# Kernel optimization log

Measured on AMD Instinct MI355X. Metric: run time of the kernel, lower is better.

## Reference

```python
import jax, jax.numpy as jnp
import numpy as np

NQ = 4          # n_qubits -> 2**4 = 16 amplitudes
NL = 3          # n_layers
TWO_PI = 2.0 * np.pi
BN_EPS = 1e-5


def _ry_batched(t):
    # t: [B] -> [B,2,2] complex64
    c, s = jnp.cos(t / 2), jnp.sin(t / 2)
    g = jnp.stack([jnp.stack([c, -s], -1), jnp.stack([s, c], -1)], -2)
    return g.astype(jnp.complex64)


def _ry(t):
    c, s = jnp.cos(t / 2), jnp.sin(t / 2)
    return jnp.stack([jnp.stack([c, -s]), jnp.stack([s, c])]).astype(jnp.complex64)


def _rz(t):
    e = jnp.stack([jnp.exp(-0.5j * t), jnp.exp(0.5j * t)]).astype(jnp.complex64)
    return jnp.diag(e)


def _apply_1q(state, gate, wire, batched):
    # state: [B,2,2,2,2]; gate: [2,2] or [B,2,2]
    s = jnp.moveaxis(state, wire + 1, -1)
    if batched:
        s = jnp.einsum('bij,b...j->b...i', gate, s)
    else:
        s = jnp.einsum('ij,...j->...i', gate, s)
    return jnp.moveaxis(s, -1, wire + 1)


def _apply_cnot(state, c, t):
    s = jnp.moveaxis(state, (c + 1, t + 1), (-2, -1))
    s = jnp.stack([s[..., 0, :], s[..., 1, ::-1]], axis=-2)  # flip target when control=1
    return jnp.moveaxis(s, (-2, -1), (c + 1, t + 1))


def _circuit(angles, weights):
    # angles: [B, NQ] float32; weights: [NL, NQ, 2]
    B = angles.shape[0]
    state = jnp.zeros((B,) + (2,) * NQ, jnp.complex64)
    state = state.at[(slice(None),) + (0,) * NQ].set(1.0)
    # input encoding RYs (per-sample angles -> batched gates)
    for i in range(NQ):
        state = _apply_1q(state, _ry_batched(angles[:, i]), i, True)
    for layer in range(NL):
        for i in range(NQ):
            state = _apply_1q(state, _ry(weights[layer, i, 0]), i, False)
            state = _apply_1q(state, _rz(weights[layer, i, 1]), i, False)
        for i in range(NQ - 1):
            state = _apply_cnot(state, i, i + 1)
        state = _apply_cnot(state, NQ - 1, 0)
    probs = jnp.abs(state) ** 2  # [B,2,2,2,2] real
    zs = []
    for i in range(NQ):
        axes = tuple(a for a in range(1, NQ + 1) if a != i + 1)
        pm = probs.sum(axis=axes)  # [B,2]
        zs.append(pm[:, 0] - pm[:, 1])
    return jnp.stack(zs, -1).astype(jnp.float32)  # [B,NQ]


def setup_inputs() -> dict:
    key = jax.random.key(0)
    ks = jax.random.split(key, 4)
    B = 524288
    x = jax.random.normal(ks[0], (B, 16), jnp.float32)
    weights = jax.random.normal(ks[1], (NL, NQ, 2), jnp.float32)
    fc_w = jax.random.normal(ks[2], (4, NQ), jnp.float32) / np.sqrt(NQ)
    fc_b = jax.random.normal(ks[3], (4,), jnp.float32) * 0.01
    gamma = jnp.ones((4,), jnp.float32)
    beta = jnp.zeros((4,), jnp.float32)
    return {"x": x, "weights": weights, "fc_w": fc_w, "fc_b": fc_b,
            "gamma": gamma, "beta": beta}


def reference(x, weights, fc_w, fc_b, gamma, beta):
    inp = x.reshape(x.shape[0], -1)[:, :NQ]
    mn, mx = inp.min(), inp.max()  # global min/max as in the torch code
    angles = TWO_PI * (inp - mn) / (mx - mn + 1e-8)
    q = _circuit(angles, weights)                # [B,4] PauliZ expvals
    out = q @ fc_w.T + fc_b                      # Linear(4,4)
    mean = out.mean(0)
    var = out.var(0)                             # biased, as torch BN training
    return gamma * (out - mean) / jnp.sqrt(var + BN_EPS) + beta
```

## Files before the change

kernel.cpp:

```cpp
#include <hip/hip_runtime.h>
#include <math.h>

#define TWO_PI_F 6.28318530717958647692f
#define BN_EPS_F 1e-5f


__device__ __forceinline__ unsigned f2key(float f) {
  unsigned u = __float_as_uint(f);
  return (u & 0x80000000u) ? ~u : (u | 0x80000000u);
}
__device__ __forceinline__ float key2f(unsigned k) {
  unsigned u = (k & 0x80000000u) ? (k ^ 0x80000000u) : ~k;
  return __uint_as_float(u);
}

__global__ void k_init(const float* __restrict__ w, float* __restrict__ wsf) {
  if (threadIdx.x == 0) {
    unsigned* wsu = (unsigned*)wsf;
    wsu[0] = 0xFFFFFFFFu;
    wsu[1] = 0x00000000u;
    for (int j = 0; j < 8; ++j) wsf[2 + j] = 0.0f;
    for (int l = 0; l < 3; ++l) {
      for (int i = 0; i < 4; ++i) {
        float th_ry = w[(l * 4 + i) * 2 + 0];
        float th_rz = w[(l * 4 + i) * 2 + 1];
        wsf[16 + l * 16 + i * 4 + 0] = cosf(0.5f * th_ry);
        wsf[16 + l * 16 + i * 4 + 1] = sinf(0.5f * th_ry);
        wsf[16 + l * 16 + i * 4 + 2] = cosf(0.5f * th_rz);
        wsf[16 + l * 16 + i * 4 + 3] = sinf(0.5f * th_rz);
      }
    }
  }
}

__global__ __launch_bounds__(256) void k_minmax(const float* __restrict__ x,
                                                unsigned* __restrict__ wsu, int B) {
  float fmn = __builtin_inff();
  float fmx = -__builtin_inff();
  for (int r = blockIdx.x * blockDim.x + threadIdx.x; r < B;
       r += gridDim.x * blockDim.x) {
    float4 v = *(const float4*)(x + (size_t)r * 16);
    fmn = fminf(fmn, fminf(fminf(v.x, v.y), fminf(v.z, v.w)));
    fmx = fmaxf(fmx, fmaxf(fmaxf(v.x, v.y), fmaxf(v.z, v.w)));
  }
#pragma unroll
  for (int d = 32; d; d >>= 1) {
    fmn = fminf(fmn, __shfl_down(fmn, d));
    fmx = fmaxf(fmx, __shfl_down(fmx, d));
  }
  __shared__ float smn[4], smx[4];
  int wave = threadIdx.x >> 6, lane = threadIdx.x & 63;
  if (lane == 0) { smn[wave] = fmn; smx[wave] = fmx; }
  __syncthreads();
  if (threadIdx.x == 0) {
    float bmn = fminf(fminf(smn[0], smn[1]), fminf(smn[2], smn[3]));
    float bmx = fmaxf(fmaxf(smx[0], smx[1]), fmaxf(smx[2], smx[3]));
    atomicMin(&wsu[0], f2key(bmn));
    atomicMax(&wsu[1], f2key(bmx));
  }
}

__global__ __launch_bounds__(256) void k_main(const float* __restrict__ x,
                                              const float* __restrict__ wsf,
                                              const float* __restrict__ fc_w,
                                              const float* __restrict__ fc_b,
                                              float* __restrict__ out, int B) {
  int b = blockIdx.x * 256 + threadIdx.x;
  const unsigned* wsu = (const unsigned*)wsf;
  float mn = key2f(wsu[0]);
  float mx = key2f(wsu[1]);
  float denom = mx - mn + 1e-8f;

  float o[4] = {0.f, 0.f, 0.f, 0.f};
  if (b < B) {
    float4 xv = *(const float4*)(x + (size_t)b * 16);
    float ang[4] = {TWO_PI_F * (xv.x - mn) / denom, TWO_PI_F * (xv.y - mn) / denom,
                    TWO_PI_F * (xv.z - mn) / denom, TWO_PI_F * (xv.w - mn) / denom};
    float cq[4], sq[4];
#pragma unroll
    for (int i = 0; i < 4; ++i) __sincosf(0.5f * ang[i], &sq[i], &cq[i]);

    float sr[16], si[16];
#pragma unroll
    for (int k = 0; k < 16; ++k) {
      sr[k] = ((k & 8) ? sq[0] : cq[0]) * ((k & 4) ? sq[1] : cq[1]) *
              ((k & 2) ? sq[2] : cq[2]) * ((k & 1) ? sq[3] : cq[3]);
      si[k] = 0.f;
    }

    const float* gt = wsf + 16;
#pragma unroll
    for (int l = 0; l < 3; ++l) {
#pragma unroll
      for (int i = 0; i < 4; ++i) {
        const int m = 8 >> i;
        float ryc = gt[l * 16 + i * 4 + 0];
        float rys = gt[l * 16 + i * 4 + 1];
        float rzc = gt[l * 16 + i * 4 + 2];
        float rzs = gt[l * 16 + i * 4 + 3];
#pragma unroll
        for (int k = 0; k < 16; ++k) {
          if (!(k & m)) {
            int k1 = k | m;
            float a0r = sr[k], a0i = si[k], a1r = sr[k1], a1i = si[k1];
            sr[k]  = ryc * a0r - rys * a1r;
            si[k]  = ryc * a0i - rys * a1i;
            sr[k1] = rys * a0r + ryc * a1r;
            si[k1] = rys * a0i + ryc * a1i;
          }
        }
#pragma unroll
        for (int k = 0; k < 16; ++k) {
          float ps = (k & m) ? rzs : -rzs;
          float r = sr[k], ii = si[k];
          sr[k] = r * rzc - ii * ps;
          si[k] = r * ps + ii * rzc;
        }
      }
#pragma unroll
      for (int c = 0; c < 4; ++c) {
        const int mc = 8 >> c;
        const int mt = 8 >> ((c + 1) & 3);
#pragma unroll
        for (int k = 0; k < 16; ++k) {
          if ((k & mc) && !(k & mt)) {
            int k2 = k | mt;
            float t;
            t = sr[k]; sr[k] = sr[k2]; sr[k2] = t;
            t = si[k]; si[k] = si[k2]; si[k2] = t;
          }
        }
      }
    }

    float z[4] = {0.f, 0.f, 0.f, 0.f};
#pragma unroll
    for (int k = 0; k < 16; ++k) {
      float p = sr[k] * sr[k] + si[k] * si[k];
#pragma unroll
      for (int i = 0; i < 4; ++i) z[i] += (k & (8 >> i)) ? -p : p;
    }
#pragma unroll
    for (int j = 0; j < 4; ++j) {
      float acc = fc_b[j];
#pragma unroll
      for (int i = 0; i < 4; ++i) acc += fc_w[j * 4 + i] * z[i];
      o[j] = acc;
    }
    *(float4*)(out + (size_t)b * 4) = make_float4(o[0], o[1], o[2], o[3]);
  }

  float vals[8] = {o[0], o[1], o[2], o[3],
                   o[0] * o[0], o[1] * o[1], o[2] * o[2], o[3] * o[3]};
#pragma unroll
  for (int j = 0; j < 8; ++j) {
#pragma unroll
    for (int d = 32; d; d >>= 1) vals[j] += __shfl_down(vals[j], d);
  }
  __shared__ float red[4][8];
  int wave = threadIdx.x >> 6, lane = threadIdx.x & 63;
  if (lane == 0) {
#pragma unroll
    for (int j = 0; j < 8; ++j) red[wave][j] = vals[j];
  }
  __syncthreads();
  if (threadIdx.x < 8) {
    float s = red[0][threadIdx.x] + red[1][threadIdx.x] + red[2][threadIdx.x] +
              red[3][threadIdx.x];
    float* stats = (float*)wsf + 2;
    atomicAdd(&stats[threadIdx.x], s);
  }
}

__global__ __launch_bounds__(256) void k_final(float* __restrict__ out,
                                               const float* __restrict__ wsf,
                                               const float* __restrict__ gamma,
                                               const float* __restrict__ beta, int B) {
  int b = blockIdx.x * 256 + threadIdx.x;
  if (b >= B) return;
  const float* stats = wsf + 2;
  float inv = 1.0f / (float)B;
  float4 v = *(float4*)(out + (size_t)b * 4);
  float vv[4] = {v.x, v.y, v.z, v.w};
  float res[4];
#pragma unroll
  for (int j = 0; j < 4; ++j) {
    float mean = stats[j] * inv;
    float var = stats[4 + j] * inv - mean * mean;
    res[j] = gamma[j] * (vv[j] - mean) * rsqrtf(var + BN_EPS_F) + beta[j];
  }
  *(float4*)(out + (size_t)b * 4) = make_float4(res[0], res[1], res[2], res[3]);
}

extern "C" void kernel_launch(void* const* d_in, const int* in_sizes, int n_in,
                              void* d_out, int out_size, void* d_ws, size_t ws_size,
                              hipStream_t stream) {
  const float* x     = (const float*)d_in[0];
  const float* w     = (const float*)d_in[1];
  const float* fc_w  = (const float*)d_in[2];
  const float* fc_b  = (const float*)d_in[3];
  const float* gamma = (const float*)d_in[4];
  const float* beta  = (const float*)d_in[5];
  float* out = (float*)d_out;
  float* wsf = (float*)d_ws;
  unsigned* wsu = (unsigned*)d_ws;
  int B = in_sizes[0] / 16;

  k_init<<<1, 64, 0, stream>>>(w, wsf);
  k_minmax<<<512, 256, 0, stream>>>(x, wsu, B);
  k_main<<<(B + 255) / 256, 256, 0, stream>>>(x, wsf, fc_w, fc_b, out, B);
  k_final<<<(B + 255) / 256, 256, 0, stream>>>(out, wsf, gamma, beta, B);
}
```

Measured before the change: 134.5 us.

## Precompute fixed circuit unitary and fold PauliZ readout into linear weights

The weight-only part of the circuit (three layers of RY/RZ and CNOT ring) is now built once in the init kernel as a 16x16 complex unitary, one column per thread. The main kernel multiplies the real product-state encoding by this unitary, about 512 FMAs against uniform workspace loads, instead of simulating every gate per sample. The PauliZ expectation and the Linear layer are folded into a 4x16 sign-weighted matrix, and the BN stat and min/max slots are padded to separate cache lines. The minmax grid is doubled, and the per-sample unitary reads rely on scalar or cached loads.

```diff
diff --git a/kernel.cpp b/kernel.cpp
--- a/kernel.cpp
+++ b/kernel.cpp
@@ -4,6 +4,13 @@
 #define TWO_PI_F 6.28318530717958647692f
 #define BN_EPS_F 1e-5f
 
+#define MINK_OFF 0
+#define MAXK_OFF 16
+#define STAT_OFF 32
+#define STAT_STRIDE 32
+#define A_OFF 288
+#define UR_OFF 384
+#define UI_OFF 640
 
 __device__ __forceinline__ unsigned f2key(float f) {
   unsigned u = __float_as_uint(f);
@@ -14,90 +21,35 @@
   return __uint_as_float(u);
 }
 
-__global__ void k_init(const float* __restrict__ w, float* __restrict__ wsf) {
-  if (threadIdx.x == 0) {
+__global__ void k_init(const float* __restrict__ w, const float* __restrict__ fc_w,
+                       float* __restrict__ wsf) {
+  int t = threadIdx.x;
+  if (t == 0) {
     unsigned* wsu = (unsigned*)wsf;
-    wsu[0] = 0xFFFFFFFFu;
-    wsu[1] = 0x00000000u;
-    for (int j = 0; j < 8; ++j) wsf[2 + j] = 0.0f;
-    for (int l = 0; l < 3; ++l) {
-      for (int i = 0; i < 4; ++i) {
-        float th_ry = w[(l * 4 + i) * 2 + 0];
-        float th_rz = w[(l * 4 + i) * 2 + 1];
-        wsf[16 + l * 16 + i * 4 + 0] = cosf(0.5f * th_ry);
-        wsf[16 + l * 16 + i * 4 + 1] = sinf(0.5f * th_ry);
-        wsf[16 + l * 16 + i * 4 + 2] = cosf(0.5f * th_rz);
-        wsf[16 + l * 16 + i * 4 + 3] = sinf(0.5f * th_rz);
-      }
-    }
-  }
-}
-
-__global__ __launch_bounds__(256) void k_minmax(const float* __restrict__ x,
-                                                unsigned* __restrict__ wsu, int B) {
-  float fmn = __builtin_inff();
-  float fmx = -__builtin_inff();
-  for (int r = blockIdx.x * blockDim.x + threadIdx.x; r < B;
-       r += gridDim.x * blockDim.x) {
-    float4 v = *(const float4*)(x + (size_t)r * 16);
-    fmn = fminf(fmn, fminf(fminf(v.x, v.y), fminf(v.z, v.w)));
-    fmx = fmaxf(fmx, fmaxf(fmaxf(v.x, v.y), fmaxf(v.z, v.w)));
-  }
-#pragma unroll
-  for (int d = 32; d; d >>= 1) {
-    fmn = fminf(fmn, __shfl_down(fmn, d));
-    fmx = fmaxf(fmx, __shfl_down(fmx, d));
-  }
-  __shared__ float smn[4], smx[4];
-  int wave = threadIdx.x >> 6, lane = threadIdx.x & 63;
-  if (lane == 0) { smn[wave] = fmn; smx[wave] = fmx; }
-  __syncthreads();
-  if (threadIdx.x == 0) {
-    float bmn = fminf(fminf(smn[0], smn[1]), fminf(smn[2], smn[3]));
-    float bmx = fmaxf(fmaxf(smx[0], smx[1]), fmaxf(smx[2], smx[3]));
-    atomicMin(&wsu[0], f2key(bmn));
-    atomicMax(&wsu[1], f2key(bmx));
-  }
-}
-
-__global__ __launch_bounds__(256) void k_main(const float* __restrict__ x,
-                                              const float* __restrict__ wsf,
-                                              const float* __restrict__ fc_w,
-                                              const float* __restrict__ fc_b,
-                                              float* __restrict__ out, int B) {
-  int b = blockIdx.x * 256 + threadIdx.x;
-  const unsigned* wsu = (const unsigned*)wsf;
-  float mn = key2f(wsu[0]);
-  float mx = key2f(wsu[1]);
-  float denom = mx - mn + 1e-8f;
-
-  float o[4] = {0.f, 0.f, 0.f, 0.f};
-  if (b < B) {
-    float4 xv = *(const float4*)(x + (size_t)b * 16);
-    float ang[4] = {TWO_PI_F * (xv.x - mn) / denom, TWO_PI_F * (xv.y - mn) / denom,
-                    TWO_PI_F * (xv.z - mn) / denom, TWO_PI_F * (xv.w - mn) / denom};
-    float cq[4], sq[4];
-#pragma unroll
-    for (int i = 0; i < 4; ++i) __sincosf(0.5f * ang[i], &sq[i], &cq[i]);
-
+    wsu[MINK_OFF] = 0xFFFFFFFFu;
+    wsu[MAXK_OFF] = 0x00000000u;
+#pragma unroll
+    for (int j = 0; j < 8; ++j) wsf[STAT_OFF + j * STAT_STRIDE] = 0.0f;
+    for (int j = 0; j < 4; ++j)
+      for (int k = 0; k < 16; ++k) {
+        float s = 0.f;
+        for (int i = 0; i < 4; ++i)
+          s += fc_w[j * 4 + i] * ((k & (8 >> i)) ? -1.f : 1.f);
+        wsf[A_OFF + j * 16 + k] = s;
+      }
+  }
+  if (t < 16) {
     float sr[16], si[16];
 #pragma unroll
-    for (int k = 0; k < 16; ++k) {
-      sr[k] = ((k & 8) ? sq[0] : cq[0]) * ((k & 4) ? sq[1] : cq[1]) *
-              ((k & 2) ? sq[2] : cq[2]) * ((k & 1) ? sq[3] : cq[3]);
-      si[k] = 0.f;
-    }
-
-    const float* gt = wsf + 16;
+    for (int k = 0; k < 16; ++k) { sr[k] = (k == t) ? 1.f : 0.f; si[k] = 0.f; }
 #pragma unroll
     for (int l = 0; l < 3; ++l) {
 #pragma unroll
       for (int i = 0; i < 4; ++i) {
         const int m = 8 >> i;
-        float ryc = gt[l * 16 + i * 4 + 0];
-        float rys = gt[l * 16 + i * 4 + 1];
-        float rzc = gt[l * 16 + i * 4 + 2];
-        float rzs = gt[l * 16 + i * 4 + 3];
+        float ryc, rys, rzc, rzs;
+        __sincosf(0.5f * w[(l * 4 + i) * 2 + 0], &rys, &ryc);
+        __sincosf(0.5f * w[(l * 4 + i) * 2 + 1], &rzs, &rzc);
 #pragma unroll
         for (int k = 0; k < 16; ++k) {
           if (!(k & m)) {
@@ -125,27 +77,98 @@
         for (int k = 0; k < 16; ++k) {
           if ((k & mc) && !(k & mt)) {
             int k2 = k | mt;
-            float t;
-            t = sr[k]; sr[k] = sr[k2]; sr[k2] = t;
-            t = si[k]; si[k] = si[k2]; si[k2] = t;
+            float tt;
+            tt = sr[k]; sr[k] = sr[k2]; sr[k2] = tt;
+            tt = si[k]; si[k] = si[k2]; si[k2] = tt;
           }
         }
       }
     }
-
-    float z[4] = {0.f, 0.f, 0.f, 0.f};
 #pragma unroll
     for (int k = 0; k < 16; ++k) {
-      float p = sr[k] * sr[k] + si[k] * si[k];
-#pragma unroll
-      for (int i = 0; i < 4; ++i) z[i] += (k & (8 >> i)) ? -p : p;
-    }
-#pragma unroll
-    for (int j = 0; j < 4; ++j) {
-      float acc = fc_b[j];
-#pragma unroll
-      for (int i = 0; i < 4; ++i) acc += fc_w[j * 4 + i] * z[i];
-      o[j] = acc;
+      wsf[UR_OFF + k * 16 + t] = sr[k];
+      wsf[UI_OFF + k * 16 + t] = si[k];
+    }
+  }
+}
+
+__global__ __launch_bounds__(256) void k_minmax(const float* __restrict__ x,
+                                                unsigned* __restrict__ wsu, int B) {
+  float fmn = __builtin_inff();
+  float fmx = -__builtin_inff();
+  for (int r = blockIdx.x * blockDim.x + threadIdx.x; r < B;
+       r += gridDim.x * blockDim.x) {
+    float4 v = *(const float4*)(x + (size_t)r * 16);
+    fmn = fminf(fmn, fminf(fminf(v.x, v.y), fminf(v.z, v.w)));
+    fmx = fmaxf(fmx, fmaxf(fmaxf(v.x, v.y), fmaxf(v.z, v.w)));
+  }
+#pragma unroll
+  for (int d = 32; d; d >>= 1) {
+    fmn = fminf(fmn, __shfl_down(fmn, d));
+    fmx = fmaxf(fmx, __shfl_down(fmx, d));
+  }
+  __shared__ float smn[4], smx[4];
+  int wave = threadIdx.x >> 6, lane = threadIdx.x & 63;
+  if (lane == 0) { smn[wave] = fmn; smx[wave] = fmx; }
+  __syncthreads();
+  if (threadIdx.x == 0) {
+    float bmn = fminf(fminf(smn[0], smn[1]), fminf(smn[2], smn[3]));
+    float bmx = fmaxf(fmaxf(smx[0], smx[1]), fmaxf(smx[2], smx[3]));
+    atomicMin(&wsu[MINK_OFF], f2key(bmn));
+    atomicMax(&wsu[MAXK_OFF], f2key(bmx));
+  }
+}
+
+__global__ __launch_bounds__(256) void k_main(const float* __restrict__ x,
+                                              const float* __restrict__ wsf,
+                                              const float* __restrict__ fc_b,
+                                              float* __restrict__ out, int B) {
+  int b = blockIdx.x * 256 + threadIdx.x;
+  const unsigned* wsu = (const unsigned*)wsf;
+  float mn = key2f(wsu[MINK_OFF]);
+  float mx = key2f(wsu[MAXK_OFF]);
+  float denom = mx - mn + 1e-8f;
+
+  float o[4] = {0.f, 0.f, 0.f, 0.f};
+  if (b < B) {
+    float4 xv = *(const float4*)(x + (size_t)b * 16);
+    float ang[4] = {TWO_PI_F * (xv.x - mn) / denom, TWO_PI_F * (xv.y - mn) / denom,
+                    TWO_PI_F * (xv.z - mn) / denom, TWO_PI_F * (xv.w - mn) / denom};
+    float cq[4], sq[4];
+#pragma unroll
+    for (int i = 0; i < 4; ++i) __sincosf(0.5f * ang[i], &sq[i], &cq[i]);
+
+    float v[16];
+#pragma unroll
+    for (int k = 0; k < 16; ++k) {
+      v[k] = ((k & 8) ? sq[0] : cq[0]) * ((k & 4) ? sq[1] : cq[1]) *
+             ((k & 2) ? sq[2] : cq[2]) * ((k & 1) ? sq[3] : cq[3]);
+    }
+
+    const float* __restrict__ Ur = wsf + UR_OFF;
+    const float* __restrict__ Ui = wsf + UI_OFF;
+    float yr[16], yi[16];
+#pragma unroll
+    for (int k = 0; k < 16; ++k) { yr[k] = 0.f; yi[k] = 0.f; }
+#pragma unroll
+    for (int a = 0; a < 16; ++a) {
+      float va = v[a];
+#pragma unroll
+      for (int k = 0; k < 16; ++k) {
+        yr[k] = fmaf(Ur[k * 16 + a], va, yr[k]);
+        yi[k] = fmaf(Ui[k * 16 + a], va, yi[k]);
+      }
+    }
+
+    const float* __restrict__ A = wsf + A_OFF;
+    o[0] = fc_b[0]; o[1] = fc_b[1]; o[2] = fc_b[2]; o[3] = fc_b[3];
+#pragma unroll
+    for (int k = 0; k < 16; ++k) {
+      float p = yr[k] * yr[k] + yi[k] * yi[k];
+      o[0] = fmaf(A[0 * 16 + k], p, o[0]);
+      o[1] = fmaf(A[1 * 16 + k], p, o[1]);
+      o[2] = fmaf(A[2 * 16 + k], p, o[2]);
+      o[3] = fmaf(A[3 * 16 + k], p, o[3]);
     }
     *(float4*)(out + (size_t)b * 4) = make_float4(o[0], o[1], o[2], o[3]);
   }
@@ -167,8 +190,7 @@
   if (threadIdx.x < 8) {
     float s = red[0][threadIdx.x] + red[1][threadIdx.x] + red[2][threadIdx.x] +
               red[3][threadIdx.x];
-    float* stats = (float*)wsf + 2;
-    atomicAdd(&stats[threadIdx.x], s);
+    atomicAdd((float*)wsf + STAT_OFF + threadIdx.x * STAT_STRIDE, s);
   }
 }
 
@@ -178,15 +200,14 @@
                                                const float* __restrict__ beta, int B) {
   int b = blockIdx.x * 256 + threadIdx.x;
   if (b >= B) return;
-  const float* stats = wsf + 2;
   float inv = 1.0f / (float)B;
   float4 v = *(float4*)(out + (size_t)b * 4);
   float vv[4] = {v.x, v.y, v.z, v.w};
   float res[4];
 #pragma unroll
   for (int j = 0; j < 4; ++j) {
-    float mean = stats[j] * inv;
-    float var = stats[4 + j] * inv - mean * mean;
+    float mean = wsf[STAT_OFF + j * STAT_STRIDE] * inv;
+    float var = wsf[STAT_OFF + (4 + j) * STAT_STRIDE] * inv - mean * mean;
     res[j] = gamma[j] * (vv[j] - mean) * rsqrtf(var + BN_EPS_F) + beta[j];
   }
   *(float4*)(out + (size_t)b * 4) = make_float4(res[0], res[1], res[2], res[3]);
@@ -206,8 +227,8 @@
   unsigned* wsu = (unsigned*)d_ws;
   int B = in_sizes[0] / 16;
 
-  k_init<<<1, 64, 0, stream>>>(w, wsf);
-  k_minmax<<<512, 256, 0, stream>>>(x, wsu, B);
-  k_main<<<(B + 255) / 256, 256, 0, stream>>>(x, wsf, fc_w, fc_b, out, B);
+  k_init<<<1, 64, 0, stream>>>(w, fc_w, wsf);
+  k_minmax<<<1024, 256, 0, stream>>>(x, wsu, B);
+  k_main<<<(B + 255) / 256, 256, 0, stream>>>(x, wsf, fc_b, out, B);
   k_final<<<(B + 255) / 256, 256, 0, stream>>>(out, wsf, gamma, beta, B);
 }
```

Result: slower. 137.6 us (+2.3%).
